# Kernel optimization log

Hardware: AMD Instinct MI355X
Metric: run time of the kernel (lower is better)

## Reference

```python
import jax, jax.numpy as jnp
import numpy as np

TOP_K = 6
N_EXPERTS = 64
ALPHA = 1e-3


def setup_inputs() -> dict:
    key = jax.random.key(0)
    k1, k2 = jax.random.split(key)
    bsz, seq_len, h = 4, 4096, 2048
    hidden_states = jax.random.normal(k1, (bsz, seq_len, h), dtype=jnp.float32)
    # kaiming_uniform_(a=sqrt(5)) on [E, h] -> bound = 1/sqrt(h)
    bound = 1.0 / np.sqrt(h)
    weight = jax.random.uniform(k2, (N_EXPERTS, h), dtype=jnp.float32, minval=-bound, maxval=bound)
    return {"hidden_states": hidden_states, "weight": weight}


def reference(hidden_states, weight):
    bsz, seq_len, h = hidden_states.shape
    E = weight.shape[0]
    x = hidden_states.reshape(-1, h)                      # [T, h], T = bsz*seq_len
    logits = jnp.einsum('th,eh->te', x, weight)           # router linear (no bias)
    scores = jax.nn.softmax(logits, axis=-1)              # [T, E]
    topk_weight, topk_idx = jax.lax.top_k(scores, TOP_K)  # [T, K]
    # norm_topk_prob renormalization
    topk_weight = topk_weight / (jnp.sum(topk_weight, axis=-1, keepdims=True) + 1e-20)
    # seq_aux auxiliary load-balancing loss (training path)
    idx_b = topk_idx.reshape(bsz, seq_len * TOP_K)        # [B, S*K]
    ce = jnp.sum(jax.nn.one_hot(idx_b, E, dtype=scores.dtype), axis=1)  # [B, E] counts
    ce = ce / (seq_len * TOP_K / E)
    mean_scores = scores.reshape(bsz, seq_len, E).mean(axis=1)          # [B, E]
    aux_loss = jnp.mean(jnp.sum(ce * mean_scores, axis=1)) * ALPHA
    return topk_idx, topk_weight, aux_loss
```

## Files before the change

kernel.cpp:

```cpp
#include <hip/hip_runtime.h>
#include <math.h>

#pragma clang fp contract(off)

#define T_TOKENS 16384
#define HDIM 2048
#define NEXP 64
#define TOPK 6
#define SEQ 4096
#define TPB 32
#define KC 64
#define WS 68
#define XS 68
#define LGS 65
#define PS 65

__device__ __forceinline__ void np_upd(const float4& w0, const float4& w1,
                                       const float4& w2, const float4& w3,
                                       const float4& x0, const float4& x1,
                                       const float4& x2, const float4& x3,
                                       float acc[4])
{
    acc[0] = w0.x*x0.x + (w1.x*x1.x + (w2.x*x2.x + (w3.x*x3.x + acc[0])));
    acc[1] = w0.y*x0.y + (w1.y*x1.y + (w2.y*x2.y + (w3.y*x3.y + acc[1])));
    acc[2] = w0.z*x0.z + (w1.z*x1.z + (w2.z*x2.z + (w3.z*x3.z + acc[2])));
    acc[3] = w0.w*x0.w + (w1.w*x1.w + (w2.w*x2.w + (w3.w*x3.w + acc[3])));
}

__global__ __launch_bounds__(256) void moe_gate_main(
    const float* __restrict__ x, const float* __restrict__ wgt,
    float* __restrict__ out, float* __restrict__ gacc)
{
    __shared__ float w_lds[NEXP * WS];
    __shared__ float x_lds[TPB * XS];
    __shared__ float lg[TPB * LGS];
    __shared__ float probs[TPB * PS];
    __shared__ float psum[4 * NEXP];
    __shared__ int   cnt[NEXP];

    const int tid  = threadIdx.x;
    const int bid  = blockIdx.x;
    const int tb   = bid * TPB;
    const int b    = tb / SEQ;

    const int lane = tid & 63;
    const int wv   = tid >> 6;
    const int le   = lane & 15;
    const int g    = lane >> 4;
    const int trow0 = wv * 8 + g * 2;

    float acc[4][2][4];
    #pragma unroll
    for (int j = 0; j < 4; ++j)
        #pragma unroll
        for (int t = 0; t < 2; ++t)
            #pragma unroll
            for (int l = 0; l < 4; ++l) acc[j][t][l] = 0.f;

    for (int c = 0; c < HDIM / KC; ++c) {
        const int k0 = c * KC;
        #pragma unroll
        for (int i = 0; i < 4; ++i) {
            int idx = i * 256 + tid;
            int e = idx >> 4, c4 = idx & 15;
            float4 v = *reinterpret_cast<const float4*>(&wgt[e * HDIM + k0 + c4 * 4]);
            *reinterpret_cast<float4*>(&w_lds[e * WS + c4 * 4]) = v;
        }
        #pragma unroll
        for (int i = 0; i < 2; ++i) {
            int idx = i * 256 + tid;
            int t = idx >> 4, c4 = idx & 15;
            float4 v = *reinterpret_cast<const float4*>(&x[(size_t)(tb + t) * HDIM + k0 + c4 * 4]);
            *reinterpret_cast<float4*>(&x_lds[t * XS + c4 * 4]) = v;
        }
        __syncthreads();

        #pragma unroll
        for (int b16 = 0; b16 < 4; ++b16) {
            const int kb = b16 * 16;
            float4 xa[2][4];
            #pragma unroll
            for (int tt = 0; tt < 2; ++tt)
                #pragma unroll
                for (int j = 0; j < 4; ++j)
                    xa[tt][j] = *reinterpret_cast<const float4*>(&x_lds[(trow0 + tt) * XS + kb + j * 4]);
            #pragma unroll
            for (int je = 0; je < 4; ++je) {
                const float* wr = &w_lds[(le + 16 * je) * WS + kb];
                float4 w0 = *reinterpret_cast<const float4*>(wr);
                float4 w1 = *reinterpret_cast<const float4*>(wr + 4);
                float4 w2 = *reinterpret_cast<const float4*>(wr + 8);
                float4 w3 = *reinterpret_cast<const float4*>(wr + 12);
                np_upd(w0, w1, w2, w3, xa[0][0], xa[0][1], xa[0][2], xa[0][3], acc[je][0]);
                np_upd(w0, w1, w2, w3, xa[1][0], xa[1][1], xa[1][2], xa[1][3], acc[je][1]);
            }
        }
        __syncthreads();
    }

    #pragma unroll
    for (int je = 0; je < 4; ++je)
        #pragma unroll
        for (int tt = 0; tt < 2; ++tt) {
            float v = (acc[je][tt][0] + acc[je][tt][1]) + (acc[je][tt][2] + acc[je][tt][3]);
            lg[(trow0 + tt) * LGS + le + 16 * je] = v;
        }
    if (tid < NEXP) cnt[tid] = 0;
    __syncthreads();

    if (tid < TPB) {
        const int t = tid;
        float mx = lg[t * LGS];
        for (int e = 1; e < NEXP; ++e) { float v = lg[t * LGS + e]; if (v > mx) mx = v; }
        for (int e = 0; e < NEXP; ++e)
            probs[t * PS + e] = expf(lg[t * LGS + e] - mx);
        float r[8];
        #pragma unroll
        for (int j = 0; j < 8; ++j) r[j] = probs[t * PS + j];
        for (int i = 8; i < 64; i += 8)
            #pragma unroll
            for (int j = 0; j < 8; ++j) r[j] += probs[t * PS + i + j];
        float S = ((r[0] + r[1]) + (r[2] + r[3])) + ((r[4] + r[5]) + (r[6] + r[7]));
        for (int e = 0; e < NEXP; ++e) probs[t * PS + e] = probs[t * PS + e] / S;
    }
    __syncthreads();

    {
        const int e = tid & 63, q = tid >> 6;
        float s = 0.f;
        for (int t = q * 8; t < q * 8 + 8; ++t) s += probs[t * PS + e];
        psum[q * 64 + e] = s;
    }
    __syncthreads();

    if (tid < TPB) {
        const int t = tid;
        const int gt = tb + t;
        float pv[TOPK]; int pi[TOPK];
        for (int r = 0; r < TOPK; ++r) {
            float bv = -1.f; int be = 0;
            for (int e = 0; e < NEXP; ++e) {
                float v = probs[t * PS + e];
                if (v > bv) { bv = v; be = e; }
            }
            probs[t * PS + be] = -1.f;
            pv[r] = bv; pi[r] = be;
            atomicAdd(&cnt[be], 1);
        }
        float wsum = pv[0];
        #pragma unroll
        for (int r = 1; r < TOPK; ++r) wsum += pv[r];
        wsum += 1e-20f;
        #pragma unroll
        for (int r = 0; r < TOPK; ++r) {
            out[(size_t)gt * TOPK + r] = (float)pi[r];
            out[(size_t)T_TOKENS * TOPK + (size_t)gt * TOPK + r] = pv[r] / wsum;
        }
    } else if (tid >= 64 && tid < 128) {
        const int e = tid - 64;
        float s = psum[e] + psum[64 + e] + psum[128 + e] + psum[192 + e];
        atomicAdd(&gacc[b * 64 + e], s);
    }
    __syncthreads();
    if (tid < NEXP) {
        atomicAdd(&gacc[256 + b * 64 + tid], (float)cnt[tid]);
    }
}

__global__ __launch_bounds__(256) void moe_gate_aux(
    const float* __restrict__ gacc, float* __restrict__ out)
{
    __shared__ float red[4];
    const int tid = threadIdx.x;
    float v = gacc[256 + tid] * gacc[tid];
    #pragma unroll
    for (int o = 32; o > 0; o >>= 1) v += __shfl_down(v, o, 64);
    if ((tid & 63) == 0) red[tid >> 6] = v;
    __syncthreads();
    if (tid == 0) {
        float tot = red[0] + red[1] + red[2] + red[3];
        const float scale = (64.0f / (4096.0f * 6.0f)) / 4096.0f;
        out[2 * T_TOKENS * TOPK] = 1e-3f * (tot * scale) * 0.25f;
    }
}

extern "C" void kernel_launch(void* const* d_in, const int* in_sizes, int n_in,
                              void* d_out, int out_size, void* d_ws, size_t ws_size,
                              hipStream_t stream) {
    const float* x   = (const float*)d_in[0];
    const float* wgt = (const float*)d_in[1];
    float* out  = (float*)d_out;
    float* gacc = (float*)d_ws;

    hipMemsetAsync(d_ws, 0, 512 * sizeof(float), stream);
    moe_gate_main<<<T_TOKENS / TPB, 256, 0, stream>>>(x, wgt, out, gacc);
    moe_gate_aux<<<1, 256, 0, stream>>>(gacc, out);
}
```

Before: 310.8 us.

## Restructure router GEMM: per-lane tokens, wave-uniform expert weights, double-buffered swizzled LDS

The block now covers 64 tokens with 512 threads. Each wave computes 8 experts, and each lane owns one token. Expert weights are read straight from global memory at wave-uniform addresses, so they can become scalar loads, replacing the LDS staging of weights. Token tiles of 128 columns are double-buffered in an XOR-swizzled LDS buffer, with register prefetch and one barrier per chunk; the post-processing buffers alias the same LDS. The aim is to cut LDS traffic and barrier overhead, at the cost of more register pressure and reliance on the scalar cache for weight reuse.

```diff
diff --git a/kernel.cpp b/kernel.cpp
--- a/kernel.cpp
+++ b/kernel.cpp
@@ -8,10 +8,9 @@
 #define NEXP 64
 #define TOPK 6
 #define SEQ 4096
-#define TPB 32
-#define KC 64
-#define WS 68
-#define XS 68
+#define TPB 64
+#define KC 128
+#define NC (HDIM / KC)
 #define LGS 65
 #define PS 65
 
@@ -27,85 +26,90 @@
     acc[3] = w0.w*x0.w + (w1.w*x1.w + (w2.w*x2.w + (w3.w*x3.w + acc[3])));
 }
 
-__global__ __launch_bounds__(256) void moe_gate_main(
+__global__ __launch_bounds__(512, 2) void moe_gate_main(
     const float* __restrict__ x, const float* __restrict__ wgt,
     float* __restrict__ out, float* __restrict__ gacc)
 {
-    __shared__ float w_lds[NEXP * WS];
-    __shared__ float x_lds[TPB * XS];
-    __shared__ float lg[TPB * LGS];
-    __shared__ float probs[TPB * PS];
-    __shared__ float psum[4 * NEXP];
-    __shared__ int   cnt[NEXP];
+    __shared__ __attribute__((aligned(16))) float xs[2 * TPB * KC];
+    float* lg    = xs;
+    float* probs = xs + 4224;
+    float* psum  = xs + 8448;
+    int*   cnt   = (int*)(xs + 8960);
 
     const int tid  = threadIdx.x;
     const int bid  = blockIdx.x;
     const int tb   = bid * TPB;
-    const int b    = tb / SEQ;
-
+    const int b    = bid >> 6;
     const int lane = tid & 63;
     const int wv   = tid >> 6;
-    const int le   = lane & 15;
-    const int g    = lane >> 4;
-    const int trow0 = wv * 8 + g * 2;
-
-    float acc[4][2][4];
-    #pragma unroll
-    for (int j = 0; j < 4; ++j)
-        #pragma unroll
-        for (int t = 0; t < 2; ++t)
-            #pragma unroll
-            for (int l = 0; l < 4; ++l) acc[j][t][l] = 0.f;
-
-    for (int c = 0; c < HDIM / KC; ++c) {
-        const int k0 = c * KC;
-        #pragma unroll
-        for (int i = 0; i < 4; ++i) {
-            int idx = i * 256 + tid;
-            int e = idx >> 4, c4 = idx & 15;
-            float4 v = *reinterpret_cast<const float4*>(&wgt[e * HDIM + k0 + c4 * 4]);
-            *reinterpret_cast<float4*>(&w_lds[e * WS + c4 * 4]) = v;
-        }
-        #pragma unroll
-        for (int i = 0; i < 2; ++i) {
-            int idx = i * 256 + tid;
-            int t = idx >> 4, c4 = idx & 15;
-            float4 v = *reinterpret_cast<const float4*>(&x[(size_t)(tb + t) * HDIM + k0 + c4 * 4]);
-            *reinterpret_cast<float4*>(&x_lds[t * XS + c4 * 4]) = v;
-        }
+
+    const int ebase = __builtin_amdgcn_readfirstlane(wv * 8);
+    const float* wbase = wgt + (size_t)ebase * HDIM;
+
+    float acc[8][4];
+    #pragma unroll
+    for (int e = 0; e < 8; ++e)
+        #pragma unroll
+        for (int l = 0; l < 4; ++l) acc[e][l] = 0.f;
+
+    size_t goff[4]; int loff[4];
+    #pragma unroll
+    for (int r = 0; r < 4; ++r) {
+        const int p   = r * 512 + tid;
+        const int row = p >> 5;
+        const int ps  = p & 31;
+        const int ls  = ps ^ (row & 7);
+        goff[r] = (size_t)(tb + row) * HDIM + ls * 4;
+        loff[r] = p * 4;
+    }
+
+    float4 tmp[4];
+    #pragma unroll
+    for (int r = 0; r < 4; ++r)
+        tmp[r] = *reinterpret_cast<const float4*>(&x[goff[r]]);
+
+    const int s16 = (lane & 7) << 4;
+    const char* xrow0 = reinterpret_cast<const char*>(xs) + lane * (KC * 4);
+
+    for (int c = 0; c < NC; ++c) {
+        float* dst = xs + (c & 1) * (TPB * KC);
+        #pragma unroll
+        for (int r = 0; r < 4; ++r)
+            *reinterpret_cast<float4*>(&dst[loff[r]]) = tmp[r];
         __syncthreads();
 
-        #pragma unroll
-        for (int b16 = 0; b16 < 4; ++b16) {
-            const int kb = b16 * 16;
-            float4 xa[2][4];
-            #pragma unroll
-            for (int tt = 0; tt < 2; ++tt)
-                #pragma unroll
-                for (int j = 0; j < 4; ++j)
-                    xa[tt][j] = *reinterpret_cast<const float4*>(&x_lds[(trow0 + tt) * XS + kb + j * 4]);
-            #pragma unroll
-            for (int je = 0; je < 4; ++je) {
-                const float* wr = &w_lds[(le + 16 * je) * WS + kb];
-                float4 w0 = *reinterpret_cast<const float4*>(wr);
-                float4 w1 = *reinterpret_cast<const float4*>(wr + 4);
-                float4 w2 = *reinterpret_cast<const float4*>(wr + 8);
-                float4 w3 = *reinterpret_cast<const float4*>(wr + 12);
-                np_upd(w0, w1, w2, w3, xa[0][0], xa[0][1], xa[0][2], xa[0][3], acc[je][0]);
-                np_upd(w0, w1, w2, w3, xa[1][0], xa[1][1], xa[1][2], xa[1][3], acc[je][1]);
+        if (c + 1 < NC) {
+            const int k0 = (c + 1) * KC;
+            #pragma unroll
+            for (int r = 0; r < 4; ++r)
+                tmp[r] = *reinterpret_cast<const float4*>(&x[goff[r] + k0]);
+        }
+
+        const char* xrow = xrow0 + (c & 1) * (TPB * KC * 4);
+        const float* wc = wbase + c * KC;
+        #pragma unroll
+        for (int kk = 0; kk < KC / 16; ++kk) {
+            float4 xa[4];
+            #pragma unroll
+            for (int j = 0; j < 4; ++j)
+                xa[j] = *reinterpret_cast<const float4*>(xrow + ((((kk * 4 + j) << 4)) ^ s16));
+            #pragma unroll
+            for (int e = 0; e < 8; ++e) {
+                const float* wr = wc + (size_t)e * HDIM + kk * 16;
+                const float4 w0 = *reinterpret_cast<const float4*>(wr);
+                const float4 w1 = *reinterpret_cast<const float4*>(wr + 4);
+                const float4 w2 = *reinterpret_cast<const float4*>(wr + 8);
+                const float4 w3 = *reinterpret_cast<const float4*>(wr + 12);
+                np_upd(w0, w1, w2, w3, xa[0], xa[1], xa[2], xa[3], acc[e]);
             }
         }
-        __syncthreads();
-    }
-
-    #pragma unroll
-    for (int je = 0; je < 4; ++je)
-        #pragma unroll
-        for (int tt = 0; tt < 2; ++tt) {
-            float v = (acc[je][tt][0] + acc[je][tt][1]) + (acc[je][tt][2] + acc[je][tt][3]);
-            lg[(trow0 + tt) * LGS + le + 16 * je] = v;
-        }
-    if (tid < NEXP) cnt[tid] = 0;
+    }
+
+    #pragma unroll
+    for (int e = 0; e < 8; ++e) {
+        float v = (acc[e][0] + acc[e][1]) + (acc[e][2] + acc[e][3]);
+        lg[lane * LGS + ebase + e] = v;
+    }
     __syncthreads();
 
     if (tid < TPB) {
@@ -122,6 +126,8 @@
             for (int j = 0; j < 8; ++j) r[j] += probs[t * PS + i + j];
         float S = ((r[0] + r[1]) + (r[2] + r[3])) + ((r[4] + r[5]) + (r[6] + r[7]));
         for (int e = 0; e < NEXP; ++e) probs[t * PS + e] = probs[t * PS + e] / S;
+    } else if (tid < 128) {
+        cnt[tid - 64] = 0;
     }
     __syncthreads();
 
@@ -156,9 +162,11 @@
             out[(size_t)gt * TOPK + r] = (float)pi[r];
             out[(size_t)T_TOKENS * TOPK + (size_t)gt * TOPK + r] = pv[r] / wsum;
         }
-    } else if (tid >= 64 && tid < 128) {
+    } else if (tid < 128) {
         const int e = tid - 64;
-        float s = psum[e] + psum[64 + e] + psum[128 + e] + psum[192 + e];
+        float s = 0.f;
+        #pragma unroll
+        for (int q = 0; q < 8; ++q) s += psum[q * 64 + e];
         atomicAdd(&gacc[b * 64 + e], s);
     }
     __syncthreads();
@@ -193,6 +201,6 @@
     float* gacc = (float*)d_ws;
 
     hipMemsetAsync(d_ws, 0, 512 * sizeof(float), stream);
-    moe_gate_main<<<T_TOKENS / TPB, 256, 0, stream>>>(x, wgt, out, gacc);
+    moe_gate_main<<<T_TOKENS / TPB, 512, 0, stream>>>(x, wgt, out, gacc);
     moe_gate_aux<<<1, 256, 0, stream>>>(gacc, out);
 }
```

Result: slower. 575.3 us (+85.1%).
